# Kernel tuning notes

Measured on AMD Instinct MI355X. Metric: run time of the kernel, lower is better.

The kernel has to match this reference:

```python
import jax, jax.numpy as jnp
import numpy as np

N = 100_000
E = 1_600_000
F_IN, D1, D2, D_EMB = 64, 32, 64, 64
NUM_GRAPHS = 16
BN_EPS = 1e-5


def _glorot(key, shape):
    fan_in, fan_out = shape[0], shape[1]
    lim = (6.0 / (fan_in + fan_out)) ** 0.5
    return jax.random.uniform(key, shape, jnp.float32, -lim, lim)


def setup_inputs() -> dict:
    key = jax.random.key(0)
    ks = jax.random.split(key, 12)
    x = jax.random.normal(ks[0], (N, F_IN), jnp.float32)
    edge_index = jax.random.randint(ks[1], (2, E), 0, N, jnp.int64)
    batch = jnp.sort(jax.random.randint(ks[2], (N,), 0, NUM_GRAPHS, jnp.int64))
    return {
        "x": x,
        "edge_index": edge_index,
        "batch": batch,
        "num_graphs": NUM_GRAPHS,
        "num_nodes": N,
        "W1a": _glorot(ks[3], (F_IN, D1)), "b1a": jnp.zeros((D1,), jnp.float32),
        "W1b": _glorot(ks[4], (D1, D2)), "b1b": jnp.zeros((D2,), jnp.float32),
        "g1": jnp.ones((D2,), jnp.float32), "be1": jnp.zeros((D2,), jnp.float32),
        "W2a": _glorot(ks[5], (D2, D2)), "b2a": jnp.zeros((D2,), jnp.float32),
        "W2b": _glorot(ks[6], (D2, D_EMB)), "b2b": jnp.zeros((D_EMB,), jnp.float32),
        "g2": jnp.ones((D_EMB,), jnp.float32), "be2": jnp.zeros((D_EMB,), jnp.float32),
    }


def _batchnorm_train(h, gamma, beta):
    mean = jnp.mean(h, axis=0)
    var = jnp.mean(jnp.square(h - mean), axis=0)  # biased var, as torch BN uses for normalization
    return (h - mean) * jax.lax.rsqrt(var + BN_EPS) * gamma + beta


def _gin_aggregate(x, src, dst, valid, n_nodes):
    # sum_{j in N(i)} x_j over valid edges only (masked scatter-add)
    msg = x[src] * valid[:, None]  # [E, D]
    return jax.ops.segment_sum(msg, dst, num_segments=n_nodes)


def reference(x, edge_index, batch, num_graphs, num_nodes,
              W1a, b1a, W1b, b1b, g1, be1,
              W2a, b2a, W2b, b2b, g2, be2):
    n_edges = edge_index.shape[1]
    per = n_edges // num_graphs
    # edge_mask: per-edge threshold g * num_nodes / num_graphs applied to both rows
    thresh = jnp.repeat(jnp.arange(num_graphs), per).astype(jnp.float32) * (num_nodes / num_graphs)
    valid = jnp.all(edge_index.astype(jnp.float32) - thresh[None, :] >= 0.0, axis=0)
    valid = valid.astype(x.dtype)
    src, dst = edge_index[0], edge_index[1]

    # GINConv 1 (eps=0): nn1(x + aggr)
    h = x + _gin_aggregate(x, src, dst, valid, num_nodes)
    h = jax.nn.relu(h @ W1a + b1a) @ W1b + b1b
    h = jax.nn.relu(h)
    h = _batchnorm_train(h, g1, be1)

    # GINConv 2
    h = h + _gin_aggregate(h, src, dst, valid, num_nodes)
    h = jax.nn.relu(h @ W2a + b2a) @ W2b + b2b
    h = jax.nn.relu(h)
    h = _batchnorm_train(h, g2, be2)

    # global_mean_pool
    sums = jax.ops.segment_sum(h, batch, num_segments=num_graphs)
    counts = jax.ops.segment_sum(jnp.ones((h.shape[0],), h.dtype), batch, num_segments=num_graphs)
    return sums / jnp.maximum(counts, 1.0)[:, None]
```

## Files before the change

### kernel.cpp

```cpp
#include <hip/hip_runtime.h>
#include <hip/hip_fp16.h>

#define NG 16
#define D 64
#define SLOT 32
#define INP 68

union HF4 { float4 f4; __half2 h2[4]; };
union HF2 { float2 f2; __half2 h2[2]; };

__global__ void to_half_kernel(const float* __restrict__ in,
                               float2* __restrict__ out, int n4) {
  int t = blockIdx.x * 256 + threadIdx.x;
  if (t < n4) {
    float4 v = ((const float4*)in)[t];
    HF2 u;
    u.h2[0] = __floats2half2_rn(v.x, v.y);
    u.h2[1] = __floats2half2_rn(v.z, v.w);
    out[t] = u.f2;
  }
}

__global__ void build_csr_kernel(const int* __restrict__ ei,
                                 int* __restrict__ fill,
                                 int* __restrict__ col,
                                 int E, int per, int tmul) {
  int e = blockIdx.x * blockDim.x + threadIdx.x;
  if (e >= E) return;
  int src = ei[e];
  int dst = ei[E + e];
  int g = e / per;
  int thr = g * tmul;
  if (src >= thr && dst >= thr) {
    int k = atomicAdd(&fill[dst], 1);
    if (k < SLOT) col[dst * SLOT + k] = src;
  }
}

__device__ __forceinline__ void tree_reduce_2x32(float* s_in, int tid) {
#pragma unroll
  for (int s = 16; s >= 1; s >>= 1) {
    if (tid < 32 * s) {
      int h = tid / (16 * s);
      int r = (tid / 16) % s;
      int qq = tid & 15;
      float4* a = (float4*)&s_in[(h * 32 + r) * INP + qq * 4];
      const float4 b = *(const float4*)&s_in[(h * 32 + r + s) * INP + qq * 4];
      a->x += b.x; a->y += b.y; a->z += b.z; a->w += b.w;
    }
    __syncthreads();
  }
}

template <int MID, bool FOLD_BN, int EPI>
__global__ __launch_bounds__(512, 2) void fused_layer_kernel(
    const float4* __restrict__ feat4,
    const int* __restrict__ col, const int* __restrict__ deg,
    const float* __restrict__ bn_sum, const float* __restrict__ bn_sq,
    const float* __restrict__ bn_gamma, const float* __restrict__ bn_beta,
    float invN,
    const float* __restrict__ Wa, const float* __restrict__ ba,
    const float* __restrict__ Wb, const float* __restrict__ bb,
    float2* __restrict__ out2,
    const int* __restrict__ batch,
    float* __restrict__ st_sum,
    float* __restrict__ st_sq,
    float* __restrict__ cnt,
    int N) {
  constexpr int NPB = 64;
  __shared__ float s_in[NPB * INP];
  __shared__ __half s_Wa[D * MID];
  __shared__ __half s_Wb[MID * D];
  __shared__ float s_bna[FOLD_BN ? D : 1];
  __shared__ float s_bnb[FOLD_BN ? D : 1];
  __shared__ int s_cnt[2];

  int tid = threadIdx.x;

  {
    const float4* wa4 = (const float4*)Wa;
    const float4* wb4 = (const float4*)Wb;
    __half2* sa2 = (__half2*)s_Wa;
    __half2* sb2 = (__half2*)s_Wb;
    constexpr int NW = D * MID / 4;
#pragma unroll
    for (int i = tid; i < NW; i += 512) {
      float4 a = wa4[i];
      float4 b = wb4[i];
      sa2[2 * i + 0] = __floats2half2_rn(a.x, a.y);
      sa2[2 * i + 1] = __floats2half2_rn(a.z, a.w);
      sb2[2 * i + 0] = __floats2half2_rn(b.x, b.y);
      sb2[2 * i + 1] = __floats2half2_rn(b.z, b.w);
    }
  }
  if (FOLD_BN && tid < D) {
    float mean = bn_sum[tid] * invN;
    float var = bn_sq[tid] * invN - mean * mean;
    float av = bn_gamma[tid] * rsqrtf(var + 1e-5f);
    s_bna[tid] = av;
    s_bnb[tid] = bn_beta[tid] - mean * av;
  }
  if (EPI == 2 && tid < 2) s_cnt[tid] = 0;
  __syncthreads();

  int base = blockIdx.x * NPB;

  {
    int slot = tid >> 3;
    int q8 = tid & 7;
    int node = base + slot;
    if (node < N) {
      int d = min(deg[node], SLOT);
      const int* cl = col + node * SLOT;
      float acc[8];
      {
        HF4 s; s.f4 = feat4[(size_t)node * 8 + q8];
#pragma unroll
        for (int i = 0; i < 4; i++) {
          float2 f = __half22float2(s.h2[i]);
          acc[2 * i] = f.x; acc[2 * i + 1] = f.y;
        }
      }
      int j = 0;
      for (; j + 8 <= d; j += 8) {
        int4 sa = *(const int4*)(cl + j);
        int4 sb = *(const int4*)(cl + j + 4);
        HF4 u0, u1, u2, u3, u4, u5, u6, u7;
        u0.f4 = feat4[(size_t)sa.x * 8 + q8];
        u1.f4 = feat4[(size_t)sa.y * 8 + q8];
        u2.f4 = feat4[(size_t)sa.z * 8 + q8];
        u3.f4 = feat4[(size_t)sa.w * 8 + q8];
        u4.f4 = feat4[(size_t)sb.x * 8 + q8];
        u5.f4 = feat4[(size_t)sb.y * 8 + q8];
        u6.f4 = feat4[(size_t)sb.z * 8 + q8];
        u7.f4 = feat4[(size_t)sb.w * 8 + q8];
#pragma unroll
        for (int i = 0; i < 4; i++) {
          float2 f0 = __half22float2(u0.h2[i]), f1 = __half22float2(u1.h2[i]);
          float2 f2 = __half22float2(u2.h2[i]), f3 = __half22float2(u3.h2[i]);
          float2 f4 = __half22float2(u4.h2[i]), f5 = __half22float2(u5.h2[i]);
          float2 f6 = __half22float2(u6.h2[i]), f7 = __half22float2(u7.h2[i]);
          acc[2 * i]     += (f0.x + f1.x + f2.x + f3.x) + (f4.x + f5.x + f6.x + f7.x);
          acc[2 * i + 1] += (f0.y + f1.y + f2.y + f3.y) + (f4.y + f5.y + f6.y + f7.y);
        }
      }
      if (j + 4 <= d) {
        int4 sa = *(const int4*)(cl + j);
        HF4 u0, u1, u2, u3;
        u0.f4 = feat4[(size_t)sa.x * 8 + q8];
        u1.f4 = feat4[(size_t)sa.y * 8 + q8];
        u2.f4 = feat4[(size_t)sa.z * 8 + q8];
        u3.f4 = feat4[(size_t)sa.w * 8 + q8];
#pragma unroll
        for (int i = 0; i < 4; i++) {
          float2 f0 = __half22float2(u0.h2[i]), f1 = __half22float2(u1.h2[i]);
          float2 f2 = __half22float2(u2.h2[i]), f3 = __half22float2(u3.h2[i]);
          acc[2 * i]     += f0.x + f1.x + f2.x + f3.x;
          acc[2 * i + 1] += f0.y + f1.y + f2.y + f3.y;
        }
        j += 4;
      }
      for (; j < d; j++) {
        HF4 u; u.f4 = feat4[(size_t)cl[j] * 8 + q8];
#pragma unroll
        for (int i = 0; i < 4; i++) {
          float2 f = __half22float2(u.h2[i]);
          acc[2 * i] += f.x; acc[2 * i + 1] += f.y;
        }
      }
      if (FOLD_BN) {
        float dp = (float)(d + 1);
        int c = q8 * 8;
#pragma unroll
        for (int i = 0; i < 8; i++)
          acc[i] = s_bna[c + i] * acc[i] + dp * s_bnb[c + i];
      }
      *(float4*)&s_in[slot * INP + q8 * 8] =
          make_float4(acc[0], acc[1], acc[2], acc[3]);
      *(float4*)&s_in[slot * INP + q8 * 8 + 4] =
          make_float4(acc[4], acc[5], acc[6], acc[7]);
    }
  }
  __syncthreads();

  int q = tid & 15;
  int r2 = tid >> 4;
  int n0 = 2 * r2, n1 = n0 + 1;
  int node0 = base + n0, node1 = base + n1;
  constexpr int C1 = MID / 16;
  float4 o0, o1;
  {
    float acc0[C1], acc1[C1];
#pragma unroll
    for (int u = 0; u < C1; u++) { acc0[u] = ba[q * C1 + u]; acc1[u] = acc0[u]; }
    const __half2* wa2 = (const __half2*)s_Wa;
#pragma unroll 4
    for (int j = 0; j < D; j++) {
      float v0 = s_in[n0 * INP + j];
      float v1 = s_in[n1 * INP + j];
#pragma unroll
      for (int u2 = 0; u2 < C1 / 2; u2++) {
        float2 w = __half22float2(wa2[(j * MID + q * C1) / 2 + u2]);
        acc0[2 * u2]     += v0 * w.x;
        acc0[2 * u2 + 1] += v0 * w.y;
        acc1[2 * u2]     += v1 * w.x;
        acc1[2 * u2 + 1] += v1 * w.y;
      }
    }
#pragma unroll
    for (int u = 0; u < C1; u++) {
      acc0[u] = fmaxf(acc0[u], 0.f);
      acc1[u] = fmaxf(acc1[u], 0.f);
    }

    const __half2* wb2 = (const __half2*)s_Wb;
    o0 = *(const float4*)(bb + q * 4);
    o1 = o0;
#pragma unroll 8
    for (int k = 0; k < MID; k++) {
      float m0 = __shfl(acc0[k % C1], k / C1, 16);
      float m1 = __shfl(acc1[k % C1], k / C1, 16);
      float2 wA = __half22float2(wb2[(k * D + q * 4) / 2]);
      float2 wB = __half22float2(wb2[(k * D + q * 4) / 2 + 1]);
      o0.x += m0 * wA.x; o0.y += m0 * wA.y; o0.z += m0 * wB.x; o0.w += m0 * wB.y;
      o1.x += m1 * wA.x; o1.y += m1 * wA.y; o1.z += m1 * wB.x; o1.w += m1 * wB.y;
    }
    o0.x = fmaxf(o0.x, 0.f); o0.y = fmaxf(o0.y, 0.f);
    o0.z = fmaxf(o0.z, 0.f); o0.w = fmaxf(o0.w, 0.f);
    o1.x = fmaxf(o1.x, 0.f); o1.y = fmaxf(o1.y, 0.f);
    o1.z = fmaxf(o1.z, 0.f); o1.w = fmaxf(o1.w, 0.f);
    if (EPI == 1) {
      if (node0 < N) {
        HF2 u;
        u.h2[0] = __floats2half2_rn(o0.x, o0.y);
        u.h2[1] = __floats2half2_rn(o0.z, o0.w);
        out2[(size_t)node0 * 16 + q] = u.f2;
      }
      if (node1 < N) {
        HF2 u;
        u.h2[0] = __floats2half2_rn(o1.x, o1.y);
        u.h2[1] = __floats2half2_rn(o1.z, o1.w);
        out2[(size_t)node1 * 16 + q] = u.f2;
      }
    }
    if (node0 >= N) o0 = make_float4(0.f, 0.f, 0.f, 0.f);
    if (node1 >= N) o1 = make_float4(0.f, 0.f, 0.f, 0.f);
  }

  if (EPI == 1) {
    __syncthreads();
    *(float4*)&s_in[r2 * INP + q * 4] =
        make_float4(o0.x + o1.x, o0.y + o1.y, o0.z + o1.z, o0.w + o1.w);
    *(float4*)&s_in[(32 + r2) * INP + q * 4] =
        make_float4(o0.x * o0.x + o1.x * o1.x, o0.y * o0.y + o1.y * o1.y,
                    o0.z * o0.z + o1.z * o1.z, o0.w * o0.w + o1.w * o1.w);
    __syncthreads();
    tree_reduce_2x32(s_in, tid);
    if (tid < D) {
      atomicAdd(&st_sum[tid], s_in[tid]);
      atomicAdd(&st_sq[tid], s_in[32 * INP + tid]);
    }
  }

  if (EPI == 2) {
    int b0 = (node0 < N) ? batch[node0] : -1;
    int b1 = (node1 < N) ? batch[node1] : -1;
    int g_lo = batch[base];
    int g_hi = batch[min(base + NPB - 1, N - 1)];

    __syncthreads();
    if (q == 0) {
      atomicAdd(&s_cnt[0], (b0 == g_lo ? 1 : 0) + (b1 == g_lo ? 1 : 0));
      if (g_hi != g_lo)
        atomicAdd(&s_cnt[1], (b0 == g_hi ? 1 : 0) + (b1 == g_hi ? 1 : 0));
    }

    float w0 = (b0 == g_lo) ? 1.f : 0.f;
    float w1 = (b1 == g_lo) ? 1.f : 0.f;
    *(float4*)&s_in[r2 * INP + q * 4] =
        make_float4(w0 * o0.x + w1 * o1.x, w0 * o0.y + w1 * o1.y,
                    w0 * o0.z + w1 * o1.z, w0 * o0.w + w1 * o1.w);
    *(float4*)&s_in[(32 + r2) * INP + q * 4] =
        make_float4(o0.x * o0.x + o1.x * o1.x, o0.y * o0.y + o1.y * o1.y,
                    o0.z * o0.z + o1.z * o1.z, o0.w * o0.w + o1.w * o1.w);
    __syncthreads();
    tree_reduce_2x32(s_in, tid);
    if (tid < D) {
      atomicAdd(&st_sum[g_lo * D + tid], s_in[tid]);
      atomicAdd(&st_sq[tid], s_in[32 * INP + tid]);
    }
    if (tid == 0) atomicAdd(&cnt[g_lo], (float)s_cnt[0]);

    if (g_hi != g_lo) {
      __syncthreads();
      float u0 = (b0 == g_hi) ? 1.f : 0.f;
      float u1 = (b1 == g_hi) ? 1.f : 0.f;
      *(float4*)&s_in[r2 * INP + q * 4] =
          make_float4(u0 * o0.x + u1 * o1.x, u0 * o0.y + u1 * o1.y,
                      u0 * o0.z + u1 * o1.z, u0 * o0.w + u1 * o1.w);
      *(float4*)&s_in[(32 + r2) * INP + q * 4] = make_float4(0.f, 0.f, 0.f, 0.f);
      __syncthreads();
      tree_reduce_2x32(s_in, tid);
      if (tid < D) atomicAdd(&st_sum[g_hi * D + tid], s_in[tid]);
      if (tid == 0) atomicAdd(&cnt[g_hi], (float)s_cnt[1]);
    }
  }
}

__global__ void final_kernel(const float* __restrict__ pool,
                             const float* __restrict__ cnt,
                             const float* __restrict__ sq,
                             const float* __restrict__ gamma,
                             const float* __restrict__ beta,
                             float invN, float* __restrict__ out) {
  int c = threadIdx.x;
  float s = 0.f;
#pragma unroll
  for (int g = 0; g < NG; g++) s += pool[g * D + c];
  float mean = s * invN;
  float var = sq[c] * invN - mean * mean;
  float a = gamma[c] * rsqrtf(var + 1e-5f);
  float b = beta[c] - mean * a;
#pragma unroll
  for (int g = 0; g < NG; g++) {
    float n = cnt[g];
    out[g * D + c] = (a * pool[g * D + c] + n * b) / fmaxf(n, 1.f);
  }
}

extern "C" void kernel_launch(void* const* d_in, const int* in_sizes, int n_in,
                              void* d_out, int out_size, void* d_ws, size_t ws_size,
                              hipStream_t stream) {
  const float* x   = (const float*)d_in[0];
  const int* ei    = (const int*)d_in[1];
  const int* batch = (const int*)d_in[2];
  const float* W1a = (const float*)d_in[5];
  const float* b1a = (const float*)d_in[6];
  const float* W1b = (const float*)d_in[7];
  const float* b1b = (const float*)d_in[8];
  const float* g1  = (const float*)d_in[9];
  const float* be1 = (const float*)d_in[10];
  const float* W2a = (const float*)d_in[11];
  const float* b2a = (const float*)d_in[12];
  const float* W2b = (const float*)d_in[13];
  const float* b2b = (const float*)d_in[14];
  const float* g2  = (const float*)d_in[15];
  const float* be2 = (const float*)d_in[16];

  int N = in_sizes[0] / D;
  int E = in_sizes[1] / 2;
  int per = E / NG;
  int tmul = N / NG;
  float invN = 1.f / (float)N;

  float* ws = (float*)d_ws;
  size_t ndh = (size_t)N * D / 2;
  float* h1h = ws;
  float* xh  = ws + ndh;
  int*   col = (int*)(ws + 2 * ndh);
  float* stats = ws + 2 * ndh + (size_t)N * SLOT;
  float* sum1 = stats;
  float* sq1  = stats + 64;
  float* pool = stats + 128;
  float* cnt  = stats + 128 + NG * D;
  float* sq2  = stats + 144 + NG * D;
  int*   fill = (int*)(stats + 208 + NG * D);

  hipMemsetAsync(stats, 0, (208 + NG * D + N) * sizeof(float), stream);

  int n4 = N * D / 4;
  to_half_kernel<<<(n4 + 255) / 256, 256, 0, stream>>>(x, (float2*)xh, n4);

  build_csr_kernel<<<(E + 255) / 256, 256, 0, stream>>>(ei, fill, col, E, per, tmul);

  int fblocks = (N + 63) / 64;

  fused_layer_kernel<32, false, 1><<<fblocks, 512, 0, stream>>>(
      (const float4*)xh, col, fill, nullptr, nullptr, nullptr, nullptr, invN,
      W1a, b1a, W1b, b1b, (float2*)h1h, nullptr, sum1, sq1, nullptr, N);

  fused_layer_kernel<64, true, 2><<<fblocks, 512, 0, stream>>>(
      (const float4*)h1h, col, fill, sum1, sq1, g1, be1, invN,
      W2a, b2a, W2b, b2b, nullptr, batch, pool, sq2, cnt, N);

  final_kernel<<<1, 64, 0, stream>>>(pool, cnt, sq2, g2, be2, invN, (float*)d_out);
}
```

Before: 270.2 us.

## Shrink fused layer blocks, stage neighbor lists in LDS, vectorize CSR build

Halves the fused GIN layer block to 256 threads handling 32 nodes, with launch bounds raised to 4 blocks per CU. Each block now copies its nodes' column lists and degrees into shared memory up front, so the gather loop reads indices from LDS. Weight reads in both matmuls are widened to one float2 load per thread, and the CSR build handles two edges per thread with int2 loads. Smaller blocks mean more blocks reload and convert the weights, and the extra shared memory may limit occupancy.

New measurement: 331.3 us. 22.6% more time.

```diff
diff --git a/kernel.cpp b/kernel.cpp
--- a/kernel.cpp
+++ b/kernel.cpp
@@ -5,6 +5,8 @@
 #define D 64
 #define SLOT 32
 #define INP 68
+#define SCOL 36
+#define NPB 32
 
 union HF4 { float4 f4; __half2 h2[4]; };
 union HF2 { float2 f2; __half2 h2[2]; };
@@ -25,27 +27,32 @@
                                  int* __restrict__ fill,
                                  int* __restrict__ col,
                                  int E, int per, int tmul) {
-  int e = blockIdx.x * blockDim.x + threadIdx.x;
+  int e = 2 * (blockIdx.x * 256 + threadIdx.x);
   if (e >= E) return;
-  int src = ei[e];
-  int dst = ei[E + e];
-  int g = e / per;
-  int thr = g * tmul;
-  if (src >= thr && dst >= thr) {
-    int k = atomicAdd(&fill[dst], 1);
-    if (k < SLOT) col[dst * SLOT + k] = src;
-  }
-}
-
-__device__ __forceinline__ void tree_reduce_2x32(float* s_in, int tid) {
-#pragma unroll
-  for (int s = 16; s >= 1; s >>= 1) {
+  int2 s2 = *(const int2*)(ei + e);
+  int2 d2 = *(const int2*)(ei + E + e);
+#pragma unroll
+  for (int i = 0; i < 2; i++) {
+    int ee = e + i;
+    int src = i ? s2.y : s2.x;
+    int dst = i ? d2.y : d2.x;
+    int thr = (ee / per) * tmul;
+    if (src >= thr && dst >= thr) {
+      int k = atomicAdd(&fill[dst], 1);
+      if (k < SLOT) col[dst * SLOT + k] = src;
+    }
+  }
+}
+
+__device__ __forceinline__ void tree_reduce_2x16(float* s_in, int tid) {
+#pragma unroll
+  for (int s = 8; s >= 1; s >>= 1) {
     if (tid < 32 * s) {
       int h = tid / (16 * s);
       int r = (tid / 16) % s;
       int qq = tid & 15;
-      float4* a = (float4*)&s_in[(h * 32 + r) * INP + qq * 4];
-      const float4 b = *(const float4*)&s_in[(h * 32 + r + s) * INP + qq * 4];
+      float4* a = (float4*)&s_in[(h * 16 + r) * INP + qq * 4];
+      const float4 b = *(const float4*)&s_in[(h * 16 + r + s) * INP + qq * 4];
       a->x += b.x; a->y += b.y; a->z += b.z; a->w += b.w;
     }
     __syncthreads();
@@ -53,7 +60,7 @@
 }
 
 template <int MID, bool FOLD_BN, int EPI>
-__global__ __launch_bounds__(512, 2) void fused_layer_kernel(
+__global__ __launch_bounds__(256, 4) void fused_layer_kernel(
     const float4* __restrict__ feat4,
     const int* __restrict__ col, const int* __restrict__ deg,
     const float* __restrict__ bn_sum, const float* __restrict__ bn_sq,
@@ -67,15 +74,17 @@
     float* __restrict__ st_sq,
     float* __restrict__ cnt,
     int N) {
-  constexpr int NPB = 64;
   __shared__ float s_in[NPB * INP];
   __shared__ __half s_Wa[D * MID];
   __shared__ __half s_Wb[MID * D];
+  __shared__ int s_col[NPB * SCOL];
+  __shared__ int s_deg[NPB];
   __shared__ float s_bna[FOLD_BN ? D : 1];
   __shared__ float s_bnb[FOLD_BN ? D : 1];
   __shared__ int s_cnt[2];
 
   int tid = threadIdx.x;
+  int base = blockIdx.x * NPB;
 
   {
     const float4* wa4 = (const float4*)Wa;
@@ -84,7 +93,7 @@
     __half2* sb2 = (__half2*)s_Wb;
     constexpr int NW = D * MID / 4;
 #pragma unroll
-    for (int i = tid; i < NW; i += 512) {
+    for (int i = tid; i < NW; i += 256) {
       float4 a = wa4[i];
       float4 b = wb4[i];
       sa2[2 * i + 0] = __floats2half2_rn(a.x, a.y);
@@ -92,6 +101,13 @@
       sb2[2 * i + 0] = __floats2half2_rn(b.x, b.y);
       sb2[2 * i + 1] = __floats2half2_rn(b.z, b.w);
     }
+    int4 c4 = ((const int4*)(col + (size_t)base * SLOT))[tid];
+    int slot = tid >> 3, j4 = tid & 7;
+    *(int4*)&s_col[slot * SCOL + j4 * 4] = c4;
+    if (tid < NPB) {
+      int node = base + tid;
+      s_deg[tid] = (node < N) ? deg[node] : 0;
+    }
   }
   if (FOLD_BN && tid < D) {
     float mean = bn_sum[tid] * invN;
@@ -103,15 +119,13 @@
   if (EPI == 2 && tid < 2) s_cnt[tid] = 0;
   __syncthreads();
 
-  int base = blockIdx.x * NPB;
-
   {
     int slot = tid >> 3;
     int q8 = tid & 7;
     int node = base + slot;
     if (node < N) {
-      int d = min(deg[node], SLOT);
-      const int* cl = col + node * SLOT;
+      int d = min(s_deg[slot], SLOT);
+      const int* cl = &s_col[slot * SCOL];
       float acc[8];
       {
         HF4 s; s.f4 = feat4[(size_t)node * 8 + q8];
@@ -193,18 +207,22 @@
     float acc0[C1], acc1[C1];
 #pragma unroll
     for (int u = 0; u < C1; u++) { acc0[u] = ba[q * C1 + u]; acc1[u] = acc0[u]; }
-    const __half2* wa2 = (const __half2*)s_Wa;
 #pragma unroll 4
     for (int j = 0; j < D; j++) {
       float v0 = s_in[n0 * INP + j];
       float v1 = s_in[n1 * INP + j];
-#pragma unroll
-      for (int u2 = 0; u2 < C1 / 2; u2++) {
-        float2 w = __half22float2(wa2[(j * MID + q * C1) / 2 + u2]);
-        acc0[2 * u2]     += v0 * w.x;
-        acc0[2 * u2 + 1] += v0 * w.y;
-        acc1[2 * u2]     += v1 * w.x;
-        acc1[2 * u2 + 1] += v1 * w.y;
+      if constexpr (C1 == 2) {
+        float2 w = __half22float2(((const __half2*)s_Wa)[j * 16 + q]);
+        acc0[0] += v0 * w.x; acc0[1] += v0 * w.y;
+        acc1[0] += v1 * w.x; acc1[1] += v1 * w.y;
+      } else {
+        HF2 u; u.f2 = ((const float2*)s_Wa)[j * 16 + q];
+        float2 wA = __half22float2(u.h2[0]);
+        float2 wB = __half22float2(u.h2[1]);
+        acc0[0] += v0 * wA.x; acc0[1] += v0 * wA.y;
+        acc0[2] += v0 * wB.x; acc0[3] += v0 * wB.y;
+        acc1[0] += v1 * wA.x; acc1[1] += v1 * wA.y;
+        acc1[2] += v1 * wB.x; acc1[3] += v1 * wB.y;
       }
     }
 #pragma unroll
@@ -213,15 +231,15 @@
       acc1[u] = fmaxf(acc1[u], 0.f);
     }
 
-    const __half2* wb2 = (const __half2*)s_Wb;
     o0 = *(const float4*)(bb + q * 4);
     o1 = o0;
 #pragma unroll 8
     for (int k = 0; k < MID; k++) {
       float m0 = __shfl(acc0[k % C1], k / C1, 16);
       float m1 = __shfl(acc1[k % C1], k / C1, 16);
-      float2 wA = __half22float2(wb2[(k * D + q * 4) / 2]);
-      float2 wB = __half22float2(wb2[(k * D + q * 4) / 2 + 1]);
+      HF2 u; u.f2 = ((const float2*)s_Wb)[k * 16 + q];
+      float2 wA = __half22float2(u.h2[0]);
+      float2 wB = __half22float2(u.h2[1]);
       o0.x += m0 * wA.x; o0.y += m0 * wA.y; o0.z += m0 * wB.x; o0.w += m0 * wB.y;
       o1.x += m1 * wA.x; o1.y += m1 * wA.y; o1.z += m1 * wB.x; o1.w += m1 * wB.y;
     }
@@ -251,14 +269,14 @@
     __syncthreads();
     *(float4*)&s_in[r2 * INP + q * 4] =
         make_float4(o0.x + o1.x, o0.y + o1.y, o0.z + o1.z, o0.w + o1.w);
-    *(float4*)&s_in[(32 + r2) * INP + q * 4] =
+    *(float4*)&s_in[(16 + r2) * INP + q * 4] =
         make_float4(o0.x * o0.x + o1.x * o1.x, o0.y * o0.y + o1.y * o1.y,
                     o0.z * o0.z + o1.z * o1.z, o0.w * o0.w + o1.w * o1.w);
     __syncthreads();
-    tree_reduce_2x32(s_in, tid);
+    tree_reduce_2x16(s_in, tid);
     if (tid < D) {
       atomicAdd(&st_sum[tid], s_in[tid]);
-      atomicAdd(&st_sq[tid], s_in[32 * INP + tid]);
+      atomicAdd(&st_sq[tid], s_in[16 * INP + tid]);
     }
   }
 
@@ -280,14 +298,14 @@
     *(float4*)&s_in[r2 * INP + q * 4] =
         make_float4(w0 * o0.x + w1 * o1.x, w0 * o0.y + w1 * o1.y,
                     w0 * o0.z + w1 * o1.z, w0 * o0.w + w1 * o1.w);
-    *(float4*)&s_in[(32 + r2) * INP + q * 4] =
+    *(float4*)&s_in[(16 + r2) * INP + q * 4] =
         make_float4(o0.x * o0.x + o1.x * o1.x, o0.y * o0.y + o1.y * o1.y,
                     o0.z * o0.z + o1.z * o1.z, o0.w * o0.w + o1.w * o1.w);
     __syncthreads();
-    tree_reduce_2x32(s_in, tid);
+    tree_reduce_2x16(s_in, tid);
     if (tid < D) {
       atomicAdd(&st_sum[g_lo * D + tid], s_in[tid]);
-      atomicAdd(&st_sq[tid], s_in[32 * INP + tid]);
+      atomicAdd(&st_sq[tid], s_in[16 * INP + tid]);
     }
     if (tid == 0) atomicAdd(&cnt[g_lo], (float)s_cnt[0]);
 
@@ -298,9 +316,9 @@
       *(float4*)&s_in[r2 * INP + q * 4] =
           make_float4(u0 * o0.x + u1 * o1.x, u0 * o0.y + u1 * o1.y,
                       u0 * o0.z + u1 * o1.z, u0 * o0.w + u1 * o1.w);
-      *(float4*)&s_in[(32 + r2) * INP + q * 4] = make_float4(0.f, 0.f, 0.f, 0.f);
+      *(float4*)&s_in[(16 + r2) * INP + q * 4] = make_float4(0.f, 0.f, 0.f, 0.f);
       __syncthreads();
-      tree_reduce_2x32(s_in, tid);
+      tree_reduce_2x16(s_in, tid);
       if (tid < D) atomicAdd(&st_sum[g_hi * D + tid], s_in[tid]);
       if (tid == 0) atomicAdd(&cnt[g_hi], (float)s_cnt[1]);
     }
@@ -371,15 +389,15 @@
   int n4 = N * D / 4;
   to_half_kernel<<<(n4 + 255) / 256, 256, 0, stream>>>(x, (float2*)xh, n4);
 
-  build_csr_kernel<<<(E + 255) / 256, 256, 0, stream>>>(ei, fill, col, E, per, tmul);
-
-  int fblocks = (N + 63) / 64;
-
-  fused_layer_kernel<32, false, 1><<<fblocks, 512, 0, stream>>>(
+  build_csr_kernel<<<(E / 2 + 255) / 256, 256, 0, stream>>>(ei, fill, col, E, per, tmul);
+
+  int fblocks = (N + NPB - 1) / NPB;
+
+  fused_layer_kernel<32, false, 1><<<fblocks, 256, 0, stream>>>(
       (const float4*)xh, col, fill, nullptr, nullptr, nullptr, nullptr, invN,
       W1a, b1a, W1b, b1b, (float2*)h1h, nullptr, sum1, sq1, nullptr, N);
 
-  fused_layer_kernel<64, true, 2><<<fblocks, 512, 0, stream>>>(
+  fused_layer_kernel<64, true, 2><<<fblocks, 256, 0, stream>>>(
       (const float4*)h1h, col, fill, sum1, sq1, g1, be1, invN,
       W2a, b2a, W2b, b2b, nullptr, batch, pool, sq2, cnt, N);
 
```
